# Kernel tuning notes

Measured on AMD Instinct MI355X. Metric: run time of the kernel, lower is better.

Reference implementation:

```python
import jax, jax.numpy as jnp
import numpy as np
from jax import lax

DN = ('NCDHW', 'OIDHW', 'NCDHW')

def conv3d(x, w, b=None):
    y = lax.conv_general_dilated(x, w, window_strides=(1, 1, 1), padding='SAME', dimension_numbers=DN)
    if b is not None:
        y = y + b[None, :, None, None, None]
    return y

def adaptive_conv(x, w):
    # x: [B,C,D,H,W]; w: [B,27,D,H,W] per-voxel 3x3x3 kernel weights
    B, C, D, H, W = x.shape
    xp = jnp.pad(x, ((0, 0), (0, 0), (1, 1), (1, 1), (1, 1)))
    out = jnp.zeros_like(x)
    idx = 0
    for i in range(3):
        for j in range(3):
            for k in range(3):
                out = out + xp[:, :, i:i + D, j:j + H, k:k + W] * w[:, idx][:, None]
                idx += 1
    return out

def setup_inputs() -> dict:
    key = jax.random.key(0)
    k1, k2, k3 = jax.random.split(key, 3)
    B, C, D, H, W = 1, 8, 128, 128, 128
    x = jax.random.normal(k1, (B, C, D, H, W), dtype=jnp.float32)
    w1 = jax.random.normal(k2, (8, 8, 3, 3, 3), dtype=jnp.float32) * 0.1
    b1 = jnp.zeros((8,), dtype=jnp.float32)
    w2 = jax.random.normal(k3, (27, 8, 3, 3, 3), dtype=jnp.float32) * 0.1
    return {"x": x, "w1": w1, "b1": b1, "w2": w2}

def reference(x, w1, b1, w2):
    # adaptive_block: per-voxel 27-tap weights from a small conv stack
    h = jax.nn.relu(conv3d(x, w1, b1))
    w = conv3d(h, w2)  # [B,27,D,H,W]
    # F.normalize(w, dim=1, p=1)
    n = jnp.sum(jnp.abs(w), axis=1, keepdims=True)
    w = w / jnp.maximum(n, 1e-12)
    out = x
    for _ in range(3):
        out = adaptive_conv(out, w)
    return out
```

## Files before the change

kernel.cpp:

```cpp
#include <hip/hip_runtime.h>
#include <hip/hip_bf16.h>

constexpr int HW2 = 16384;
constexpr int DHW = 2097152;

constexpr int PKG = 13;
constexpr int XT  = 130;

typedef short bf16x8 __attribute__((ext_vector_type(8)));
typedef float f32x4  __attribute__((ext_vector_type(4)));

__device__ inline unsigned short f2b(float f) {
  __hip_bfloat16 h = __float2bfloat16(f);
  return *(unsigned short*)&h;
}
__device__ inline float b2f(unsigned short u) {
  __hip_bfloat16 h = *(__hip_bfloat16*)&u;
  return __bfloat162float(h);
}

__global__ __launch_bounds__(256) void k_prep(
    const float* __restrict__ w1, const float* __restrict__ w2,
    unsigned short* __restrict__ Wpack2, unsigned short* __restrict__ Wpack1,
    float* __restrict__ g_ti, float* __restrict__ g_xi) {
  int i = blockIdx.x * 256 + threadIdx.x;
  if (i < 9216) {
    int j = i & 7;
    int lane = (i >> 3) & 63;
    int Mt = (i >> 9) & 1;
    int g2 = i >> 10;
    int s = g2 % 3, dx = g2 / 3;
    int oc = Mt * 16 + (lane & 15);
    int kr = s * 32 + (lane >> 4) * 8 + j;
    int ci = kr & 7, g = kr >> 3;
    float w = 0.f;
    if (oc < 27 && (g & 3) < 3) {
      int dzr = g >> 2, dyr = g & 3;
      w = w2[(oc * 8 + ci) * 27 + dzr * 9 + dyr * 3 + dx];
    }
    Wpack2[i] = f2b(w);
  }
  int jj = i - 9216;
  if (jj >= 0 && jj < 4608) {
    int j = jj & 7;
    int lane = (jj >> 3) & 63;
    int g2 = jj >> 9;
    int s = g2 % 3, dx = g2 / 3;
    int oc = lane & 15;
    int kr = s * 32 + (lane >> 4) * 8 + j;
    int ci = kr & 7, g = kr >> 3;
    float w = 0.f;
    if (oc < 8 && (g & 3) < 3) {
      int dzr = g >> 2, dyr = g & 3;
      w = w1[(oc * 8 + ci) * 27 + dzr * 9 + dyr * 3 + dx];
    }
    Wpack1[jj] = f2b(w);
  }
  int gg = i - 13824;
  if (gg >= 0 && gg < 32) {
    float* p = (gg < 8)  ? (g_ti - 8 + gg)
             : (gg < 16) ? (g_ti + (size_t)8 * DHW + (gg - 8))
             : (gg < 24) ? (g_xi - 8 + (gg - 16))
                         : (g_xi + (size_t)8 * DHW + (gg - 24));
    *p = 0.f;
  }
}

__global__ __launch_bounds__(256) void k_xpose(
    const float* __restrict__ x, unsigned short* __restrict__ xb,
    float* __restrict__ xi) {
  int idx = blockIdx.x * 256 + threadIdx.x;
  float f[8];
  unsigned v[4];
#pragma unroll
  for (int p = 0; p < 4; ++p) {
    f[2 * p]     = x[(size_t)(2 * p) * DHW + idx];
    f[2 * p + 1] = x[(size_t)(2 * p + 1) * DHW + idx];
    unsigned lo = f2b(f[2 * p]);
    unsigned hi = f2b(f[2 * p + 1]);
    v[p] = lo | (hi << 16);
  }
  ((uint4*)xb)[idx] = make_uint4(v[0], v[1], v[2], v[3]);
  float4* xo = (float4*)(xi + (size_t)idx * 8);
  xo[0] = make_float4(f[0], f[1], f[2], f[3]);
  xo[1] = make_float4(f[4], f[5], f[6], f[7]);
}

#define STAGE_ROWS(srcp)                                                   \
  {                                                                        \
    if (tid < 24) {                                                        \
      int gh = tid >> 1, xih = (tid & 1) ? 129 : 0;                        \
      dst[xih * PKG + gh] = make_uint4(0u, 0u, 0u, 0u);                    \
    }                                                                      \
    const int gg = tid >> 7;                                               \
    const int xi_ = (tid & 127) + 1;                                       \
    const int xg_ = xi_ - 1;                                               \
    uint4 sv[6];                                                           \
    bool vld[6];                                                           \
    _Pragma("unroll")                                                      \
    for (int it = 0; it < 6; ++it) {                                       \
      const int g = gg + it * 2;                                           \
      const int dz = g >> 2, dy = g & 3;                                   \
      const int z = z0 + dz - 1, y = y0 + dy - 1;                          \
      vld[it] = (dy < 3) & ((unsigned)z < 128u) & ((unsigned)y < 128u);    \
      const int zz = vld[it] ? z : z0, yy = vld[it] ? y : y0;              \
      sv[it] = (srcp)[(zz * 128 + yy) * 128 + xg_];                        \
    }                                                                      \
    _Pragma("unroll")                                                      \
    for (int it = 0; it < 6; ++it) {                                       \
      const int g = gg + it * 2;                                           \
      uint4 v = vld[it] ? sv[it] : make_uint4(0u, 0u, 0u, 0u);             \
      dst[xi_ * PKG + g] = v;                                              \
    }                                                                      \
  }

__global__ __launch_bounds__(256) void k_conv1m(
    const unsigned short* __restrict__ xb,
    const unsigned short* __restrict__ Wpack1,
    const float* __restrict__ b1, unsigned short* __restrict__ hb) {
  __shared__ __align__(16) unsigned short T[XT * PKG * 8];
  const int tid  = threadIdx.x;
  const int lane = tid & 63;
  const int wv   = tid >> 6;
  const int logical = (blockIdx.x & 7) * 2048 + (blockIdx.x >> 3);
  const int z0 = logical >> 7;
  const int y0 = logical & 127;

  bf16x8 wf[3][3];
  {
    const bf16x8* wp = (const bf16x8*)Wpack1;
#pragma unroll
    for (int dx = 0; dx < 3; ++dx)
#pragma unroll
      for (int s = 0; s < 3; ++s)
        wf[dx][s] = wp[(dx * 3 + s) * 64 + lane];
  }

  const uint4* src = (const uint4*)xb;
  uint4* dst = (uint4*)T;
  STAGE_ROWS(src);
  __syncthreads();

  f32x4 acc[2];
#pragma unroll
  for (int nt = 0; nt < 2; ++nt) acc[nt] = (f32x4){0.f, 0.f, 0.f, 0.f};

  const int n = lane & 15;
  const int q = lane >> 4;
  const int xbase = wv * 32 + n;

#pragma unroll
  for (int dx = 0; dx < 3; ++dx) {
#pragma unroll
    for (int s = 0; s < 3; ++s) {
      bf16x8 bfr[2];
#pragma unroll
      for (int nt = 0; nt < 2; ++nt) {
        int off = ((xbase + nt * 16 + dx) * PKG + (s * 4 + q)) * 8;
        bfr[nt] = *(const bf16x8*)&T[off];
      }
#pragma unroll
      for (int nt = 0; nt < 2; ++nt)
        acc[nt] = __builtin_amdgcn_mfma_f32_16x16x32_bf16(
            wf[dx][s], bfr[nt], acc[nt], 0, 0, 0);
    }
  }

  const int voxrow = (z0 * 128 + y0) * 128;
  if (q < 2) {
#pragma unroll
    for (int nt = 0; nt < 2; ++nt) {
      const int vox = voxrow + wv * 32 + nt * 16 + n;
      ushort4 o;
      o.x = f2b(fmaxf(acc[nt][0] + b1[q * 4 + 0], 0.f));
      o.y = f2b(fmaxf(acc[nt][1] + b1[q * 4 + 1], 0.f));
      o.z = f2b(fmaxf(acc[nt][2] + b1[q * 4 + 2], 0.f));
      o.w = f2b(fmaxf(acc[nt][3] + b1[q * 4 + 3], 0.f));
      *(ushort4*)(hb + (size_t)vox * 8 + q * 4) = o;
    }
  }
}

__global__ __launch_bounds__(256) void k_conv2(
    const unsigned short* __restrict__ hb,
    const unsigned short* __restrict__ Wpack2,
    unsigned short* __restrict__ wn) {
  __shared__ __align__(16) unsigned short T[XT * PKG * 8];
  const int tid  = threadIdx.x;
  const int lane = tid & 63;
  const int wv   = tid >> 6;
  const int logical = (blockIdx.x & 7) * 2048 + (blockIdx.x >> 3);
  const int z0 = logical >> 7;
  const int y0 = logical & 127;

  bf16x8 wf[3][3][2];
  {
    const bf16x8* wp = (const bf16x8*)Wpack2;
#pragma unroll
    for (int dx = 0; dx < 3; ++dx)
#pragma unroll
      for (int s = 0; s < 3; ++s)
#pragma unroll
        for (int mt = 0; mt < 2; ++mt)
          wf[dx][s][mt] = wp[((dx * 3 + s) * 2 + mt) * 64 + lane];
  }

  const uint4* src = (const uint4*)hb;
  uint4* dst = (uint4*)T;
  STAGE_ROWS(src);
  __syncthreads();

  f32x4 acc[2][2];
#pragma unroll
  for (int nt = 0; nt < 2; ++nt)
#pragma unroll
    for (int mt = 0; mt < 2; ++mt) acc[nt][mt] = (f32x4){0.f, 0.f, 0.f, 0.f};

  const int n = lane & 15;
  const int q = lane >> 4;
  const int xbase = wv * 32 + n;

#pragma unroll
  for (int dx = 0; dx < 3; ++dx) {
#pragma unroll
    for (int s = 0; s < 3; ++s) {
      bf16x8 bfr[2];
#pragma unroll
      for (int nt = 0; nt < 2; ++nt) {
        int off = ((xbase + nt * 16 + dx) * PKG + (s * 4 + q)) * 8;
        bfr[nt] = *(const bf16x8*)&T[off];
      }
#pragma unroll
      for (int mt = 0; mt < 2; ++mt)
#pragma unroll
        for (int nt = 0; nt < 2; ++nt)
          acc[nt][mt] = __builtin_amdgcn_mfma_f32_16x16x32_bf16(
              wf[dx][s][mt], bfr[nt], acc[nt][mt], 0, 0, 0);
    }
  }

  const int voxrow = (z0 * 128 + y0) * 128;
#pragma unroll
  for (int nt = 0; nt < 2; ++nt) {
    float ns = 0.f;
#pragma unroll
    for (int r = 0; r < 4; ++r) ns += fabsf(acc[nt][0][r]);
#pragma unroll
    for (int r = 0; r < 4; ++r) {
      int oc = 16 + q * 4 + r;
      ns += (oc < 27) ? fabsf(acc[nt][1][r]) : 0.f;
    }
    ns += __shfl_xor(ns, 16);
    ns += __shfl_xor(ns, 32);
    float sc = 1.f / fmaxf(ns, 1e-12f);
    const int vox = voxrow + wv * 32 + nt * 16 + n;
#pragma unroll
    for (int r = 0; r < 4; ++r) {
      int oc = q * 4 + r;
      wn[(size_t)oc * DHW + vox] = f2b(acc[nt][0][r] * sc);
    }
#pragma unroll
    for (int r = 0; r < 4; ++r) {
      int oc = 16 + q * 4 + r;
      if (oc < 27)
        wn[(size_t)oc * DHW + vox] = f2b(acc[nt][1][r] * sc);
    }
  }
}

__device__ inline int swzb(int off) { return off ^ (((off >> 7) & 7) << 4); }

template <int FINAL>
__global__ __launch_bounds__(256, 2) void k_adapt4(
    const float* __restrict__ in, const unsigned short* __restrict__ wn,
    float* __restrict__ out) {
  __shared__ __align__(16) char S[16 * 4224];
  const int tid = threadIdx.x;
  const int logical = (blockIdx.x & 7) * 512 + (blockIdx.x >> 3);
  const int ty = logical & 63, tz = logical >> 6;
  const int y0 = ty * 2, z0 = tz * 2;

  uint4 stg[16];
#pragma unroll
  for (int c = 0; c < 16; ++c) {
    const int zs = min(max(z0 - 1 + (c >> 2), 0), 127);
    const int ys = min(max(y0 - 1 + (c & 3), 0), 127);
    stg[c] = ((const uint4*)(in + (size_t)(zs * 128 + ys) * 1024))[tid];
  }
  {
    const int off = swzb(32 + tid * 16);
#pragma unroll
    for (int c = 0; c < 16; ++c)
      *(uint4*)(S + c * 4224 + off) = stg[c];
  }
  if (tid < 64) {
    const int row = tid >> 2, part = tid & 3;
    const int off = (part < 2) ? part * 16 : (4128 + (part - 2) * 16);
    *(uint4*)(S + row * 4224 + swzb(off)) = make_uint4(0u, 0u, 0u, 0u);
  }
  __syncthreads();

  const int wv = tid >> 6, lane = tid & 63;
  const int zl = wv >> 1, yl = wv & 1;
  const int zout = z0 + zl, yout = y0 + yl;
  const int xg = lane * 2;
  const int vox0 = (zout * 128 + yout) * 128 + xg;

  int soff[4][2];
#pragma unroll
  for (int p = 0; p < 4; ++p)
#pragma unroll
    for (int h = 0; h < 2; ++h)
      soff[p][h] = swzb((xg + p) * 32 + h * 16);

  f32x4 a0A = (f32x4){0.f, 0.f, 0.f, 0.f};
  f32x4 a0B = (f32x4){0.f, 0.f, 0.f, 0.f};
  f32x4 a1A = (f32x4){0.f, 0.f, 0.f, 0.f};
  f32x4 a1B = (f32x4){0.f, 0.f, 0.f, 0.f};

#pragma unroll
  for (int g = 0; g < 9; ++g) {
    const int dzp = g / 3, dyp = g % 3;
    const char* R = S + ((zl + dzp) * 4 + (yl + dyp)) * 4224;
    f32x4 W[4][2];
#pragma unroll
    for (int p = 0; p < 4; ++p)
#pragma unroll
      for (int h = 0; h < 2; ++h)
        W[p][h] = *(const f32x4*)(R + soff[p][h]);
    const bool val = ((unsigned)(zout + dzp - 1) < 128u) &
                     ((unsigned)(yout + dyp - 1) < 128u);
#pragma unroll
    for (int dxi = 0; dxi < 3; ++dxi) {
      const unsigned u =
          *(const unsigned*)(wn + (size_t)(g * 3 + dxi) * DHW + vox0);
      const float wl = val ? b2f((unsigned short)(u & 0xffffu)) : 0.f;
      const float wh = val ? b2f((unsigned short)(u >> 16)) : 0.f;
#pragma unroll
      for (int c = 0; c < 4; ++c) {
        a0A[c] = fmaf(W[dxi][0][c], wl, a0A[c]);
        a0B[c] = fmaf(W[dxi][1][c], wl, a0B[c]);
        a1A[c] = fmaf(W[dxi + 1][0][c], wh, a1A[c]);
        a1B[c] = fmaf(W[dxi + 1][1][c], wh, a1B[c]);
      }
    }
  }

  if (FINAL) {
#pragma unroll
    for (int c = 0; c < 4; ++c) {
      *(float2*)(out + (size_t)c * DHW + vox0) = make_float2(a0A[c], a1A[c]);
      *(float2*)(out + (size_t)(c + 4) * DHW + vox0) =
          make_float2(a0B[c], a1B[c]);
    }
  } else {
    f32x4* op = (f32x4*)(out + (size_t)vox0 * 8);
    op[0] = a0A;
    op[1] = a0B;
    op[2] = a1A;
    op[3] = a1B;
  }
}

extern "C" void kernel_launch(void* const* d_in, const int* in_sizes, int n_in,
                              void* d_out, int out_size, void* d_ws, size_t ws_size,
                              hipStream_t stream) {
  const float* x  = (const float*)d_in[0];
  const float* w1 = (const float*)d_in[1];
  const float* b1 = (const float*)d_in[2];
  const float* w2 = (const float*)d_in[3];
  float* out = (float*)d_out;

  char* ws = (char*)d_ws;
  unsigned short* xb = (unsigned short*)ws;
  unsigned short* hb = (unsigned short*)(ws + (size_t)8 * DHW * 2);
  float* ti = (float*)(ws + 256);
  unsigned short* wn = (unsigned short*)(ws + (size_t)16 * DHW * 2 + 4096);
  float* xi = (float*)(ws + (size_t)16 * DHW * 2 + 4096 +
                       (size_t)27 * DHW * 2 + 8192);
  unsigned short* Wpack2 =
      (unsigned short*)((char*)xi + (size_t)8 * DHW * 4 + 16384);
  unsigned short* Wpack1 = Wpack2 + 9216;

  dim3 blk(256);
  k_prep<<<55, blk, 0, stream>>>(w1, w2, Wpack2, Wpack1, ti, xi);
  k_xpose<<<DHW / 256, blk, 0, stream>>>(x, xb, xi);
  k_conv1m<<<128 * 128, blk, 0, stream>>>(xb, Wpack1, b1, hb);
  k_conv2<<<128 * 128, blk, 0, stream>>>(hb, Wpack2, wn);
  k_adapt4<0><<<64 * 64, blk, 0, stream>>>(xi, wn, ti);
  k_adapt4<0><<<64 * 64, blk, 0, stream>>>(ti, wn, xi);
  k_adapt4<1><<<64 * 64, blk, 0, stream>>>(xi, wn, out);
}
```

Baseline: 388.4 us.

## Compute two y-rows per block in conv kernels and prefetch adaptive weights

The two MFMA conv kernels now process two adjacent y rows per block. They stage a 3x4 halo of z/y rows into shared memory, with a zeroed pad slot, and reuse the staged slices and weight fragments for both output rows. This halves the grid and cuts redundant halo loads, at the cost of more accumulator registers, so the kernels get occupancy hints in launch_bounds. The adaptive kernel also issues all 27 per-voxel weight loads up front, before the shared-memory store and barrier, to overlap that global latency with staging, which raises register pressure.

```diff
diff --git a/kernel.cpp b/kernel.cpp
--- a/kernel.cpp
+++ b/kernel.cpp
@@ -86,11 +86,16 @@
   xo[1] = make_float4(f[4], f[5], f[6], f[7]);
 }
 
-#define STAGE_ROWS(srcp)                                                   \
+#define STAGE_ROWS2(srcp)                                                  \
   {                                                                        \
-    if (tid < 24) {                                                        \
-      int gh = tid >> 1, xih = (tid & 1) ? 129 : 0;                        \
-      dst[xih * PKG + gh] = make_uint4(0u, 0u, 0u, 0u);                    \
+    if (tid < 154) {                                                       \
+      if (tid < 130) {                                                     \
+        dst[tid * PKG + 12] = make_uint4(0u, 0u, 0u, 0u);                  \
+      } else {                                                             \
+        int k = tid - 130;                                                 \
+        int sl = k >> 1, xih = (k & 1) ? 129 : 0;                          \
+        dst[xih * PKG + sl] = make_uint4(0u, 0u, 0u, 0u);                  \
+      }                                                                    \
     }                                                                      \
     const int gg = tid >> 7;                                               \
     const int xi_ = (tid & 127) + 1;                                       \
@@ -100,9 +105,9 @@
     _Pragma("unroll")                                                      \
     for (int it = 0; it < 6; ++it) {                                       \
       const int g = gg + it * 2;                                           \
-      const int dz = g >> 2, dy = g & 3;                                   \
-      const int z = z0 + dz - 1, y = y0 + dy - 1;                          \
-      vld[it] = (dy < 3) & ((unsigned)z < 128u) & ((unsigned)y < 128u);    \
+      const int dz = g >> 2, ry = g & 3;                                   \
+      const int z = z0 + dz - 1, y = y0 + ry - 1;                          \
+      vld[it] = ((unsigned)z < 128u) & ((unsigned)y < 128u);               \
       const int zz = vld[it] ? z : z0, yy = vld[it] ? y : y0;              \
       sv[it] = (srcp)[(zz * 128 + yy) * 128 + xg_];                        \
     }                                                                      \
@@ -114,7 +119,7 @@
     }                                                                      \
   }
 
-__global__ __launch_bounds__(256) void k_conv1m(
+__global__ __launch_bounds__(256, 3) void k_conv1m(
     const unsigned short* __restrict__ xb,
     const unsigned short* __restrict__ Wpack1,
     const float* __restrict__ b1, unsigned short* __restrict__ hb) {
@@ -122,9 +127,9 @@
   const int tid  = threadIdx.x;
   const int lane = tid & 63;
   const int wv   = tid >> 6;
-  const int logical = (blockIdx.x & 7) * 2048 + (blockIdx.x >> 3);
-  const int z0 = logical >> 7;
-  const int y0 = logical & 127;
+  const int logical = (blockIdx.x & 7) * 1024 + (blockIdx.x >> 3);
+  const int z0 = logical >> 6;
+  const int y0 = (logical & 63) * 2;
 
   bf16x8 wf[3][3];
   {
@@ -138,12 +143,14 @@
 
   const uint4* src = (const uint4*)xb;
   uint4* dst = (uint4*)T;
-  STAGE_ROWS(src);
+  STAGE_ROWS2(src);
   __syncthreads();
 
-  f32x4 acc[2];
-#pragma unroll
-  for (int nt = 0; nt < 2; ++nt) acc[nt] = (f32x4){0.f, 0.f, 0.f, 0.f};
+  f32x4 acc[2][2];
+#pragma unroll
+  for (int r = 0; r < 2; ++r)
+#pragma unroll
+    for (int nt = 0; nt < 2; ++nt) acc[r][nt] = (f32x4){0.f, 0.f, 0.f, 0.f};
 
   const int n = lane & 15;
   const int q = lane >> 4;
@@ -153,35 +160,42 @@
   for (int dx = 0; dx < 3; ++dx) {
 #pragma unroll
     for (int s = 0; s < 3; ++s) {
-      bf16x8 bfr[2];
+      bf16x8 bfr[2][2];
+#pragma unroll
+      for (int r = 0; r < 2; ++r)
+#pragma unroll
+        for (int nt = 0; nt < 2; ++nt) {
+          int off = ((xbase + nt * 16 + dx) * PKG + (s * 4 + q + r)) * 8;
+          bfr[r][nt] = *(const bf16x8*)&T[off];
+        }
+#pragma unroll
+      for (int r = 0; r < 2; ++r)
+#pragma unroll
+        for (int nt = 0; nt < 2; ++nt)
+          acc[r][nt] = __builtin_amdgcn_mfma_f32_16x16x32_bf16(
+              wf[dx][s], bfr[r][nt], acc[r][nt], 0, 0, 0);
+    }
+  }
+
+  if (q < 2) {
+#pragma unroll
+    for (int r = 0; r < 2; ++r) {
+      const int voxrow = (z0 * 128 + y0 + r) * 128;
 #pragma unroll
       for (int nt = 0; nt < 2; ++nt) {
-        int off = ((xbase + nt * 16 + dx) * PKG + (s * 4 + q)) * 8;
-        bfr[nt] = *(const bf16x8*)&T[off];
+        const int vox = voxrow + wv * 32 + nt * 16 + n;
+        ushort4 o;
+        o.x = f2b(fmaxf(acc[r][nt][0] + b1[q * 4 + 0], 0.f));
+        o.y = f2b(fmaxf(acc[r][nt][1] + b1[q * 4 + 1], 0.f));
+        o.z = f2b(fmaxf(acc[r][nt][2] + b1[q * 4 + 2], 0.f));
+        o.w = f2b(fmaxf(acc[r][nt][3] + b1[q * 4 + 3], 0.f));
+        *(ushort4*)(hb + (size_t)vox * 8 + q * 4) = o;
       }
-#pragma unroll
-      for (int nt = 0; nt < 2; ++nt)
-        acc[nt] = __builtin_amdgcn_mfma_f32_16x16x32_bf16(
-            wf[dx][s], bfr[nt], acc[nt], 0, 0, 0);
-    }
-  }
-
-  const int voxrow = (z0 * 128 + y0) * 128;
-  if (q < 2) {
-#pragma unroll
-    for (int nt = 0; nt < 2; ++nt) {
-      const int vox = voxrow + wv * 32 + nt * 16 + n;
-      ushort4 o;
-      o.x = f2b(fmaxf(acc[nt][0] + b1[q * 4 + 0], 0.f));
-      o.y = f2b(fmaxf(acc[nt][1] + b1[q * 4 + 1], 0.f));
-      o.z = f2b(fmaxf(acc[nt][2] + b1[q * 4 + 2], 0.f));
-      o.w = f2b(fmaxf(acc[nt][3] + b1[q * 4 + 3], 0.f));
-      *(ushort4*)(hb + (size_t)vox * 8 + q * 4) = o;
-    }
-  }
-}
-
-__global__ __launch_bounds__(256) void k_conv2(
+    }
+  }
+}
+
+__global__ __launch_bounds__(256, 2) void k_conv2(
     const unsigned short* __restrict__ hb,
     const unsigned short* __restrict__ Wpack2,
     unsigned short* __restrict__ wn) {
@@ -189,9 +203,9 @@
   const int tid  = threadIdx.x;
   const int lane = tid & 63;
   const int wv   = tid >> 6;
-  const int logical = (blockIdx.x & 7) * 2048 + (blockIdx.x >> 3);
-  const int z0 = logical >> 7;
-  const int y0 = logical & 127;
+  const int logical = (blockIdx.x & 7) * 1024 + (blockIdx.x >> 3);
+  const int z0 = logical >> 6;
+  const int y0 = (logical & 63) * 2;
 
   bf16x8 wf[3][3][2];
   {
@@ -207,14 +221,17 @@
 
   const uint4* src = (const uint4*)hb;
   uint4* dst = (uint4*)T;
-  STAGE_ROWS(src);
+  STAGE_ROWS2(src);
   __syncthreads();
 
-  f32x4 acc[2][2];
-#pragma unroll
-  for (int nt = 0; nt < 2; ++nt)
-#pragma unroll
-    for (int mt = 0; mt < 2; ++mt) acc[nt][mt] = (f32x4){0.f, 0.f, 0.f, 0.f};
+  f32x4 acc[2][2][2];
+#pragma unroll
+  for (int r = 0; r < 2; ++r)
+#pragma unroll
+    for (int nt = 0; nt < 2; ++nt)
+#pragma unroll
+      for (int mt = 0; mt < 2; ++mt)
+        acc[r][nt][mt] = (f32x4){0.f, 0.f, 0.f, 0.f};
 
   const int n = lane & 15;
   const int q = lane >> 4;
@@ -224,46 +241,53 @@
   for (int dx = 0; dx < 3; ++dx) {
 #pragma unroll
     for (int s = 0; s < 3; ++s) {
-      bf16x8 bfr[2];
-#pragma unroll
-      for (int nt = 0; nt < 2; ++nt) {
-        int off = ((xbase + nt * 16 + dx) * PKG + (s * 4 + q)) * 8;
-        bfr[nt] = *(const bf16x8*)&T[off];
+      bf16x8 bfr[2][2];
+#pragma unroll
+      for (int r = 0; r < 2; ++r)
+#pragma unroll
+        for (int nt = 0; nt < 2; ++nt) {
+          int off = ((xbase + nt * 16 + dx) * PKG + (s * 4 + q + r)) * 8;
+          bfr[r][nt] = *(const bf16x8*)&T[off];
+        }
+#pragma unroll
+      for (int r = 0; r < 2; ++r)
+#pragma unroll
+        for (int mt = 0; mt < 2; ++mt)
+#pragma unroll
+          for (int nt = 0; nt < 2; ++nt)
+            acc[r][nt][mt] = __builtin_amdgcn_mfma_f32_16x16x32_bf16(
+                wf[dx][s][mt], bfr[r][nt], acc[r][nt][mt], 0, 0, 0);
+    }
+  }
+
+#pragma unroll
+  for (int r = 0; r < 2; ++r) {
+    const int voxrow = (z0 * 128 + y0 + r) * 128;
+#pragma unroll
+    for (int nt = 0; nt < 2; ++nt) {
+      float ns = 0.f;
+#pragma unroll
+      for (int rr = 0; rr < 4; ++rr) ns += fabsf(acc[r][nt][0][rr]);
+#pragma unroll
+      for (int rr = 0; rr < 4; ++rr) {
+        int oc = 16 + q * 4 + rr;
+        ns += (oc < 27) ? fabsf(acc[r][nt][1][rr]) : 0.f;
       }
-#pragma unroll
-      for (int mt = 0; mt < 2; ++mt)
-#pragma unroll
-        for (int nt = 0; nt < 2; ++nt)
-          acc[nt][mt] = __builtin_amdgcn_mfma_f32_16x16x32_bf16(
-              wf[dx][s][mt], bfr[nt], acc[nt][mt], 0, 0, 0);
-    }
-  }
-
-  const int voxrow = (z0 * 128 + y0) * 128;
-#pragma unroll
-  for (int nt = 0; nt < 2; ++nt) {
-    float ns = 0.f;
-#pragma unroll
-    for (int r = 0; r < 4; ++r) ns += fabsf(acc[nt][0][r]);
-#pragma unroll
-    for (int r = 0; r < 4; ++r) {
-      int oc = 16 + q * 4 + r;
-      ns += (oc < 27) ? fabsf(acc[nt][1][r]) : 0.f;
-    }
-    ns += __shfl_xor(ns, 16);
-    ns += __shfl_xor(ns, 32);
-    float sc = 1.f / fmaxf(ns, 1e-12f);
-    const int vox = voxrow + wv * 32 + nt * 16 + n;
-#pragma unroll
-    for (int r = 0; r < 4; ++r) {
-      int oc = q * 4 + r;
-      wn[(size_t)oc * DHW + vox] = f2b(acc[nt][0][r] * sc);
-    }
-#pragma unroll
-    for (int r = 0; r < 4; ++r) {
-      int oc = 16 + q * 4 + r;
-      if (oc < 27)
-        wn[(size_t)oc * DHW + vox] = f2b(acc[nt][1][r] * sc);
+      ns += __shfl_xor(ns, 16);
+      ns += __shfl_xor(ns, 32);
+      float sc = 1.f / fmaxf(ns, 1e-12f);
+      const int vox = voxrow + wv * 32 + nt * 16 + n;
+#pragma unroll
+      for (int rr = 0; rr < 4; ++rr) {
+        int oc = q * 4 + rr;
+        wn[(size_t)oc * DHW + vox] = f2b(acc[r][nt][0][rr] * sc);
+      }
+#pragma unroll
+      for (int rr = 0; rr < 4; ++rr) {
+        int oc = 16 + q * 4 + rr;
+        if (oc < 27)
+          wn[(size_t)oc * DHW + vox] = f2b(acc[r][nt][1][rr] * sc);
+      }
     }
   }
 }
@@ -280,32 +304,38 @@
   const int ty = logical & 63, tz = logical >> 6;
   const int y0 = ty * 2, z0 = tz * 2;
 
-  uint4 stg[16];
-#pragma unroll
-  for (int c = 0; c < 16; ++c) {
-    const int zs = min(max(z0 - 1 + (c >> 2), 0), 127);
-    const int ys = min(max(y0 - 1 + (c & 3), 0), 127);
-    stg[c] = ((const uint4*)(in + (size_t)(zs * 128 + ys) * 1024))[tid];
-  }
-  {
-    const int off = swzb(32 + tid * 16);
-#pragma unroll
-    for (int c = 0; c < 16; ++c)
-      *(uint4*)(S + c * 4224 + off) = stg[c];
-  }
-  if (tid < 64) {
-    const int row = tid >> 2, part = tid & 3;
-    const int off = (part < 2) ? part * 16 : (4128 + (part - 2) * 16);
-    *(uint4*)(S + row * 4224 + swzb(off)) = make_uint4(0u, 0u, 0u, 0u);
-  }
-  __syncthreads();
-
   const int wv = tid >> 6, lane = tid & 63;
   const int zl = wv >> 1, yl = wv & 1;
   const int zout = z0 + zl, yout = y0 + yl;
   const int xg = lane * 2;
   const int vox0 = (zout * 128 + yout) * 128 + xg;
 
+  uint4 stg[16];
+#pragma unroll
+  for (int c = 0; c < 16; ++c) {
+    const int zs = min(max(z0 - 1 + (c >> 2), 0), 127);
+    const int ys = min(max(y0 - 1 + (c & 3), 0), 127);
+    stg[c] = ((const uint4*)(in + (size_t)(zs * 128 + ys) * 1024))[tid];
+  }
+
+  unsigned wnv[27];
+#pragma unroll
+  for (int k = 0; k < 27; ++k)
+    wnv[k] = *(const unsigned*)(wn + (size_t)k * DHW + vox0);
+
+  {
+    const int off = swzb(32 + tid * 16);
+#pragma unroll
+    for (int c = 0; c < 16; ++c)
+      *(uint4*)(S + c * 4224 + off) = stg[c];
+  }
+  if (tid < 64) {
+    const int row = tid >> 2, part = tid & 3;
+    const int off = (part < 2) ? part * 16 : (4128 + (part - 2) * 16);
+    *(uint4*)(S + row * 4224 + swzb(off)) = make_uint4(0u, 0u, 0u, 0u);
+  }
+  __syncthreads();
+
   int soff[4][2];
 #pragma unroll
   for (int p = 0; p < 4; ++p)
@@ -332,8 +362,7 @@
                      ((unsigned)(yout + dyp - 1) < 128u);
 #pragma unroll
     for (int dxi = 0; dxi < 3; ++dxi) {
-      const unsigned u =
-          *(const unsigned*)(wn + (size_t)(g * 3 + dxi) * DHW + vox0);
+      const unsigned u = wnv[g * 3 + dxi];
       const float wl = val ? b2f((unsigned short)(u & 0xffffu)) : 0.f;
       const float wh = val ? b2f((unsigned short)(u >> 16)) : 0.f;
 #pragma unroll
@@ -385,8 +414,8 @@
   dim3 blk(256);
   k_prep<<<55, blk, 0, stream>>>(w1, w2, Wpack2, Wpack1, ti, xi);
   k_xpose<<<DHW / 256, blk, 0, stream>>>(x, xb, xi);
-  k_conv1m<<<128 * 128, blk, 0, stream>>>(xb, Wpack1, b1, hb);
-  k_conv2<<<128 * 128, blk, 0, stream>>>(hb, Wpack2, wn);
+  k_conv1m<<<128 * 64, blk, 0, stream>>>(xb, Wpack1, b1, hb);
+  k_conv2<<<128 * 64, blk, 0, stream>>>(hb, Wpack2, wn);
   k_adapt4<0><<<64 * 64, blk, 0, stream>>>(xi, wn, ti);
   k_adapt4<0><<<64 * 64, blk, 0, stream>>>(ti, wn, xi);
   k_adapt4<1><<<64 * 64, blk, 0, stream>>>(xi, wn, out);
```

New measurement: 353.3 us. 1.1x faster.
